# Performance work log

Measured on AMD Instinct MI355X. Metric: run time of the kernel, lower is better.

The kernel has to match this reference:

```python
import jax, jax.numpy as jnp
import numpy as np

B, L, DMQ, DMV = 8, 1024, 512, 512
H, DK, DV, DOUT = 8, 64, 64, 512
EPS = 1e-6


def _layer_norm(x, gamma, beta):
    # LayerNorm over last dim (size H*DK or H*DV), eps=1e-6
    mu = jnp.mean(x, axis=-1, keepdims=True)
    var = jnp.mean(jnp.square(x - mu), axis=-1, keepdims=True)
    return (x - mu) * jax.lax.rsqrt(var + EPS) * gamma + beta


def setup_inputs() -> dict:
    key = jax.random.key(0)
    ks = jax.random.split(key, 20)
    s = 0.02
    return {
        "q": jax.random.normal(ks[0], (B, L, DMQ), jnp.float32),
        "k": jax.random.normal(ks[1], (B, L, DMV), jnp.float32),
        "v": jax.random.normal(ks[2], (B, L, DMV), jnp.float32),
        "Wq": jax.random.normal(ks[3], (DMQ, H * DK), jnp.float32) * s,
        "bq": jnp.zeros((H * DK,), jnp.float32),
        "Wk": jax.random.normal(ks[4], (DMV, H * DK), jnp.float32) * s,
        "bk": jnp.zeros((H * DK,), jnp.float32),
        "Wv": jax.random.normal(ks[5], (DMV, H * DV), jnp.float32) * s,
        "bv": jnp.zeros((H * DV,), jnp.float32),
        "g_q": jnp.ones((H * DK,), jnp.float32),
        "be_q": jnp.zeros((H * DK,), jnp.float32),
        "g_k": jnp.ones((H * DK,), jnp.float32),
        "be_k": jnp.zeros((H * DK,), jnp.float32),
        "g_v": jnp.ones((H * DV,), jnp.float32),
        "be_v": jnp.zeros((H * DV,), jnp.float32),
        "W1": jax.random.normal(ks[6], (H * DV, H * DV), jnp.float32) * s,
        "b1": jnp.zeros((H * DV,), jnp.float32),
        "W2": jax.random.normal(ks[7], (H * DV, DOUT), jnp.float32) * s,
        "b2": jnp.zeros((DOUT,), jnp.float32),
    }


def reference(q, k, v, Wq, bq, Wk, bk, Wv, bv, g_q, be_q, g_k, be_k, g_v, be_v, W1, b1, W2, b2):
    b, lq = q.shape[0], q.shape[1]
    qp = q @ Wq + bq                       # [B, Lq, H*DK]
    kp = k @ Wk + bk                       # [B, Lk, H*DK]
    vp = v @ Wv + bv                       # [B, Lv, H*DV]
    residual = qp.reshape(b, lq, H, DK)
    qn = _layer_norm(qp, g_q, be_q).reshape(b, lq, H, DK)
    kn = _layer_norm(kp, g_k, be_k).reshape(b, -1, H, DK)
    vn = _layer_norm(vp, g_v, be_v).reshape(b, -1, H, DV)
    # scaled dot-product attention (mask=None path)
    scores = jnp.einsum("bqhd,bkhd->bhqk", qn, kn) / jnp.sqrt(jnp.float32(DK))
    attn = jax.nn.softmax(scores, axis=-1)
    out = jnp.einsum("bhqk,bkhd->bqhd", attn, vn).reshape(b, lq, H * DV)
    # 2-layer FFN head: fc1 (ReLU) then fc2
    h = jax.nn.relu(out @ W1 + b1)
    out = h @ W2 + b2                      # [B, Lq, DOUT]
    return (out, residual)
```

## Files before the change

kernel.cpp:

```cpp
#include <hip/hip_runtime.h>
#include <hip/hip_bf16.h>
#include <stdint.h>

typedef unsigned short u16;
typedef __attribute__((ext_vector_type(8))) short bf16x8;
typedef __attribute__((ext_vector_type(4))) float f32x4;
typedef __attribute__((ext_vector_type(16))) float f32x16;

#define NR 8192
#define DM 512
#define NH 8
#define HD 64
#define LQ 1024

#define QSCALE (0.125f * 1.4426950408889634f)
#define SOFF 16.0f

__device__ __forceinline__ u16 f2b(float f) {
    union { float f; uint32_t u; } v; v.f = f;
    uint32_t r = v.u + 0x7fffu + ((v.u >> 16) & 1u);
    return (u16)(r >> 16);
}
__device__ __forceinline__ uint32_t pk2(float lo, float hi) {
    __hip_bfloat162 h = __float22bfloat162_rn(make_float2(lo, hi));
    union { __hip_bfloat162 h; uint32_t u; } c; c.h = h;
    return c.u;
}

__global__ __launch_bounds__(256)
void conv3_kernel(const float* __restrict__ q, const float* __restrict__ k,
                  const float* __restrict__ v, u16* __restrict__ qo,
                  u16* __restrict__ ko, u16* __restrict__ vo)
{
    const int y = blockIdx.y;
    const float* in = y == 0 ? q : y == 1 ? k : v;
    u16* out = y == 0 ? qo : y == 1 ? ko : vo;
    const int i = blockIdx.x * 256 + threadIdx.x;
    const float4* p = (const float4*)in + (size_t)i * 2;
    float4 a = p[0], b = p[1];
    uint4 o;
    o.x = pk2(a.x, a.y);
    o.y = pk2(a.z, a.w);
    o.z = pk2(b.x, b.y);
    o.w = pk2(b.z, b.w);
    ((uint4*)out)[i] = o;
}

__global__ __launch_bounds__(256)
void wt5_kernel(const float* __restrict__ W0, const float* __restrict__ W1,
                const float* __restrict__ W2, const float* __restrict__ W3,
                const float* __restrict__ W4,
                u16* __restrict__ T0, u16* __restrict__ T1, u16* __restrict__ T2,
                u16* __restrict__ T3, u16* __restrict__ T4)
{
    const int z = blockIdx.z;
    const float* W = z == 0 ? W0 : z == 1 ? W1 : z == 2 ? W2 : z == 3 ? W3 : W4;
    u16* Wt = z == 0 ? T0 : z == 1 ? T1 : z == 2 ? T2 : z == 3 ? T3 : T4;

    __shared__ float S[64][65];
    const int k0 = blockIdx.x * 64, n0 = blockIdx.y * 64;
    #pragma unroll
    for (int p = 0; p < 16; ++p) {
        int idx = threadIdx.x + p * 256;
        int r = idx >> 6, c = idx & 63;
        S[r][c] = W[(size_t)(k0 + r) * DM + n0 + c];
    }
    __syncthreads();
    #pragma unroll
    for (int p = 0; p < 16; ++p) {
        int idx = threadIdx.x + p * 256;
        int r = idx >> 6, c = idx & 63;
        Wt[(size_t)(n0 + r) * DM + k0 + c] = f2b(S[c][r]);
    }
}

__global__ __launch_bounds__(256)
void vt_kernel(const u16* __restrict__ vn, u16* __restrict__ vt)
{
    __shared__ u16 S[64][82];
    const int lt = blockIdx.x, bh = blockIdx.y;
    const int b = bh >> 3, h = bh & 7;
    const int t = threadIdx.x;
    {
        const int r = t >> 2, dc = (t & 3) * 16;
        const u16* src = vn + (size_t)(b * LQ + lt * 64 + r) * DM + h * HD + dc;
        *(uint4*)&S[r][dc]     = *(const uint4*)(src);
        *(uint4*)&S[r][dc + 8] = *(const uint4*)(src + 8);
    }
    __syncthreads();
    {
        const int d = t >> 2, lc = (t & 3) * 16;
        u16 tmp[16];
        #pragma unroll
        for (int e = 0; e < 16; ++e) tmp[e] = S[lc + e][d];
        u16* dst = vt + (((size_t)bh * HD + d) << 10) + lt * 64 + lc;
        *(uint4*)dst       = *(uint4*)&tmp[0];
        *(uint4*)(dst + 8) = *(uint4*)&tmp[8];
    }
}

__global__ __launch_bounds__(256)
void ln3_kernel(const float* __restrict__ Pq, const float* __restrict__ Pk,
                const float* __restrict__ Pv,
                const float* __restrict__ gq, const float* __restrict__ bq,
                const float* __restrict__ gk, const float* __restrict__ bk,
                const float* __restrict__ gv, const float* __restrict__ bv,
                u16* __restrict__ oq, u16* __restrict__ ok, u16* __restrict__ ov)
{
    const int y = blockIdx.y;
    const float* P  = y == 0 ? Pq : y == 1 ? Pk : Pv;
    const float* gm = y == 0 ? gq : y == 1 ? gk : gv;
    const float* be = y == 0 ? bq : y == 1 ? bk : bv;
    u16* out = y == 0 ? oq : y == 1 ? ok : ov;
    const float scale = y == 0 ? QSCALE : 1.f;

    const int row = blockIdx.x, t = threadIdx.x;
    const size_t off = (size_t)row * DM + t * 2;
    float2 v = *(const float2*)(P + off);
    float s = v.x + v.y, s2 = v.x * v.x + v.y * v.y;
    #pragma unroll
    for (int o = 32; o; o >>= 1) { s += __shfl_down(s, o); s2 += __shfl_down(s2, o); }
    __shared__ float ss[4], ss2[4];
    if ((t & 63) == 0) { ss[t >> 6] = s; ss2[t >> 6] = s2; }
    __syncthreads();
    float S = ss[0] + ss[1] + ss[2] + ss[3];
    float S2 = ss2[0] + ss2[1] + ss2[2] + ss2[3];
    float mu = S * (1.f / DM);
    float var = S2 * (1.f / DM) - mu * mu;
    float rs = rsqrtf(var + 1e-6f);
    float g0 = gm[t * 2] * scale, g1 = gm[t * 2 + 1] * scale;
    float b0 = be[t * 2] * scale, b1 = be[t * 2 + 1] * scale;
    float o0 = (v.x - mu) * rs * g0 + b0;
    float o1 = (v.y - mu) * rs * g1 + b1;
    *(uint32_t*)(out + off) = pk2(o0, o1);
}

template<bool RELU, bool OUT_BF16>
__device__ __forceinline__
void gemm_body(const u16* __restrict__ A, const u16* __restrict__ Bt,
               const float* __restrict__ bias, void* __restrict__ Cout)
{
    __shared__ u16 Al[4 * 128 * 8];
    __shared__ u16 Bl[4 * 128 * 8];
    const int t = threadIdx.x;
    const int w = t >> 6, l = t & 63;
    const int m0 = blockIdx.x * 128, n0 = blockIdx.y * 128;
    const int sg = w & 3, sr = (w >> 2) * 64;
    const int wm = w >> 2, wn = w & 3;

    const u16* Ap = A  + (size_t)(m0 + sr + l) * DM + sg * 8;
    const u16* Bp = Bt + (size_t)(n0 + sr + l) * DM + sg * 8;
    const int su = (sg * 128 + sr + l) * 8;

    uint4 ga = *(const uint4*)Ap;
    uint4 gb = *(const uint4*)Bp;

    f32x4 acc[4][2];
    #pragma unroll
    for (int mi = 0; mi < 4; ++mi)
        #pragma unroll
        for (int ni = 0; ni < 2; ++ni)
            acc[mi][ni] = {0.f, 0.f, 0.f, 0.f};

    for (int kb = 0; kb < DM / 32; ++kb) {
        __syncthreads();
        *(uint4*)&Al[su] = ga;
        *(uint4*)&Bl[su] = gb;
        if (kb + 1 < DM / 32) {
            ga = *(const uint4*)(Ap + (kb + 1) * 32);
            gb = *(const uint4*)(Bp + (kb + 1) * 32);
        }
        __syncthreads();
        bf16x8 af[4], bfr[2];
        #pragma unroll
        for (int mi = 0; mi < 4; ++mi)
            af[mi] = *(const bf16x8*)&Al[((l >> 4) * 128 + wm * 64 + mi * 16 + (l & 15)) * 8];
        #pragma unroll
        for (int ni = 0; ni < 2; ++ni)
            bfr[ni] = *(const bf16x8*)&Bl[((l >> 4) * 128 + wn * 32 + ni * 16 + (l & 15)) * 8];
        #pragma unroll
        for (int mi = 0; mi < 4; ++mi)
            #pragma unroll
            for (int ni = 0; ni < 2; ++ni)
                acc[mi][ni] = __builtin_amdgcn_mfma_f32_16x16x32_bf16(af[mi], bfr[ni], acc[mi][ni], 0, 0, 0);
    }

    const int cq = l >> 4, cr = l & 15;
    #pragma unroll
    for (int mi = 0; mi < 4; ++mi) {
        const int row = m0 + wm * 64 + mi * 16 + cq * 4;
        #pragma unroll
        for (int ni = 0; ni < 2; ++ni) {
            const int col = n0 + wn * 32 + ni * 16 + cr;
            const float bb = bias[col];
            #pragma unroll
            for (int j = 0; j < 4; ++j) {
                float vv = acc[mi][ni][j] + bb;
                if (RELU) vv = fmaxf(vv, 0.f);
                if (OUT_BF16) ((u16*)Cout)[(size_t)(row + j) * DM + col] = f2b(vv);
                else          ((float*)Cout)[(size_t)(row + j) * DM + col] = vv;
            }
        }
    }
}

template<bool RELU, bool OUT_BF16>
__global__ __launch_bounds__(512)
void mfma_gemm_kernel(const u16* __restrict__ A, const u16* __restrict__ Bt,
                      const float* __restrict__ bias, void* __restrict__ Cout)
{
    gemm_body<RELU, OUT_BF16>(A, Bt, bias, Cout);
}

__global__ __launch_bounds__(512)
void gemm_qkv_kernel(const u16* __restrict__ qbf, const u16* __restrict__ kbf,
                     const u16* __restrict__ vbf,
                     const u16* __restrict__ WqT, const u16* __restrict__ WkT,
                     const u16* __restrict__ WvT,
                     const float* __restrict__ bq, const float* __restrict__ bk,
                     const float* __restrict__ bv,
                     float* __restrict__ res, float* __restrict__ kp,
                     float* __restrict__ vp)
{
    const int z = blockIdx.z;
    const u16* A    = z == 0 ? qbf : z == 1 ? kbf : vbf;
    const u16* Bt   = z == 0 ? WqT : z == 1 ? WkT : WvT;
    const float* bb = z == 0 ? bq  : z == 1 ? bk  : bv;
    void* C         = z == 0 ? (void*)res : z == 1 ? (void*)kp : (void*)vp;
    gemm_body<false, false>(A, Bt, bb, C);
}

__global__ __launch_bounds__(256, 3)
void attn_mfma_kernel(const u16* __restrict__ qn, const u16* __restrict__ kn,
                      const u16* __restrict__ vt, u16* __restrict__ ab)
{
    __shared__ u16 Kl[2][8 * 64 * 8];
    __shared__ u16 Vl[2][8 * 64 * 8];
    __shared__ u16 Pl[4][8 * 32 * 8];

    const int t = threadIdx.x;
    const int w = t >> 6, l = t & 63;
    const int hi = l >> 5, ln = l & 31;

    const int bid = blockIdx.x;
    const int slot = bid >> 3;
    const int bh = (bid & 7) + 8 * (slot & 7);
    const int qt = slot >> 3;
    const int b = bh >> 3, h = bh & 7;

    const size_t bbase = (size_t)b * LQ * DM + h * HD;
    const int q0 = qt * 128 + w * 32;

    bf16x8 qf[4];
    {
        const u16* qp = qn + bbase + (size_t)(q0 + ln) * DM + hi * 8;
        #pragma unroll
        for (int c = 0; c < 4; ++c)
            qf[c] = *(const bf16x8*)(qp + c * 16);
    }

    const u16* Kg = kn + bbase + (size_t)(t & 63) * DM + (t >> 6) * 8;
    const u16* Vg = vt + (((size_t)bh * HD + (t >> 3)) << 10) + (t & 7) * 8;
    const int svu1 = ((t & 7) * 64 + (t >> 3)) * 8;
    const int svu2 = ((t & 7) * 64 + 32 + (t >> 3)) * 8;
    u16* Pw = &Pl[w][0];

    f32x16 oa0, oa1;
    #pragma unroll
    for (int r = 0; r < 16; ++r) { oa0[r] = 0.f; oa1[r] = 0.f; }
    float lsum = 0.f;

    *(uint4*)&Kl[0][t * 8]         = *(const uint4*)Kg;
    *(uint4*)&Kl[0][(t + 256) * 8] = *(const uint4*)(Kg + 32);
    *(uint4*)&Vl[0][svu1]          = *(const uint4*)Vg;
    *(uint4*)&Vl[0][svu2]          = *(const uint4*)(Vg + (32 << 10));
    uint4 ka1 = *(const uint4*)(Kg + (size_t)64 * DM);
    uint4 ka2 = *(const uint4*)(Kg + (size_t)64 * DM + 32);
    uint4 va1 = *(const uint4*)(Vg + 64);
    uint4 va2 = *(const uint4*)(Vg + (32 << 10) + 64);
    int cur = 0;

    for (int kt = 0; kt < 16; ++kt) {
        __syncthreads();

        f32x16 sa0, sa1;
        #pragma unroll
        for (int r = 0; r < 16; ++r) { sa0[r] = -SOFF; sa1[r] = -SOFF; }
        #pragma unroll
        for (int c = 0; c < 4; ++c) {
            bf16x8 k0 = *(const bf16x8*)&Kl[cur][((c * 2 + hi) * 64 + ln) * 8];
            bf16x8 k1 = *(const bf16x8*)&Kl[cur][((c * 2 + hi) * 64 + 32 + ln) * 8];
            sa0 = __builtin_amdgcn_mfma_f32_32x32x16_bf16(k0, qf[c], sa0, 0, 0, 0);
            sa1 = __builtin_amdgcn_mfma_f32_32x32x16_bf16(k1, qf[c], sa1, 0, 0, 0);
        }

        if (kt < 15) {
            *(uint4*)&Kl[cur ^ 1][t * 8]         = ka1;
            *(uint4*)&Kl[cur ^ 1][(t + 256) * 8] = ka2;
            *(uint4*)&Vl[cur ^ 1][svu1]          = va1;
            *(uint4*)&Vl[cur ^ 1][svu2]          = va2;
            if (kt < 14) {
                ka1 = *(const uint4*)(Kg + (size_t)(kt + 2) * 64 * DM);
                ka2 = *(const uint4*)(Kg + (size_t)(kt + 2) * 64 * DM + 32);
                va1 = *(const uint4*)(Vg + (kt + 2) * 64);
                va2 = *(const uint4*)(Vg + (32 << 10) + (kt + 2) * 64);
            }
        }

        #pragma unroll
        for (int r = 0; r < 16; ++r) {
            sa0[r] = __builtin_amdgcn_exp2f(sa0[r]);
            sa1[r] = __builtin_amdgcn_exp2f(sa1[r]);
            lsum += sa0[r] + sa1[r];
        }

        #pragma unroll
        for (int g0 = 0; g0 < 4; ++g0) {
            uint2 w0, w1;
            w0.x = pk2(sa0[4 * g0],     sa0[4 * g0 + 1]);
            w0.y = pk2(sa0[4 * g0 + 2], sa0[4 * g0 + 3]);
            w1.x = pk2(sa1[4 * g0],     sa1[4 * g0 + 1]);
            w1.y = pk2(sa1[4 * g0 + 2], sa1[4 * g0 + 3]);
            *(uint2*)&Pw[(g0 * 32 + ln) * 8 + 4 * hi]       = w0;
            *(uint2*)&Pw[((g0 + 4) * 32 + ln) * 8 + 4 * hi] = w1;
        }

        #pragma unroll
        for (int ks = 0; ks < 4; ++ks) {
            bf16x8 pa = *(const bf16x8*)&Pw[((ks * 2 + hi) * 32 + ln) * 8];
            bf16x8 v0 = *(const bf16x8*)&Vl[cur][((ks * 2 + hi) * 64 + ln) * 8];
            bf16x8 v1 = *(const bf16x8*)&Vl[cur][((ks * 2 + hi) * 64 + 32 + ln) * 8];
            oa0 = __builtin_amdgcn_mfma_f32_32x32x16_bf16(v0, pa, oa0, 0, 0, 0);
            oa1 = __builtin_amdgcn_mfma_f32_32x32x16_bf16(v1, pa, oa1, 0, 0, 0);
        }
        cur ^= 1;
    }

    lsum += __shfl_xor(lsum, 32, 64);
    const float rinv = 1.f / lsum;
    u16* op = ab + (size_t)(b * LQ + q0 + ln) * DM + h * HD;
    #pragma unroll
    for (int g = 0; g < 4; ++g) {
        uint2 s0, s1;
        s0.x = pk2(oa0[4 * g] * rinv, oa0[4 * g + 1] * rinv);
        s0.y = pk2(oa0[4 * g + 2] * rinv, oa0[4 * g + 3] * rinv);
        s1.x = pk2(oa1[4 * g] * rinv, oa1[4 * g + 1] * rinv);
        s1.y = pk2(oa1[4 * g + 2] * rinv, oa1[4 * g + 3] * rinv);
        *(uint2*)(op + 8 * g + 4 * hi)      = s0;
        *(uint2*)(op + 32 + 8 * g + 4 * hi) = s1;
    }
}

extern "C" void kernel_launch(void* const* d_in, const int* in_sizes, int n_in,
                              void* d_out, int out_size, void* d_ws, size_t ws_size,
                              hipStream_t stream)
{
    const float* q    = (const float*)d_in[0];
    const float* k    = (const float*)d_in[1];
    const float* v    = (const float*)d_in[2];
    const float* Wq   = (const float*)d_in[3];
    const float* bq   = (const float*)d_in[4];
    const float* Wk   = (const float*)d_in[5];
    const float* bk   = (const float*)d_in[6];
    const float* Wv   = (const float*)d_in[7];
    const float* bv   = (const float*)d_in[8];
    const float* g_q  = (const float*)d_in[9];
    const float* be_q = (const float*)d_in[10];
    const float* g_k  = (const float*)d_in[11];
    const float* be_k = (const float*)d_in[12];
    const float* g_v  = (const float*)d_in[13];
    const float* be_v = (const float*)d_in[14];
    const float* W1   = (const float*)d_in[15];
    const float* b1   = (const float*)d_in[16];
    const float* W2   = (const float*)d_in[17];
    const float* b2   = (const float*)d_in[18];

    float* outp = (float*)d_out;
    float* res  = outp + (size_t)NR * DM;

    char* wsb = (char*)d_ws;
    const size_t MB = 1024 * 1024;
    float* kp  = (float*)(wsb);
    float* vp  = (float*)(wsb + 16 * MB);
    u16* qbf = (u16*)(wsb + 32 * MB);
    u16* kbf = (u16*)(wsb + 40 * MB);
    u16* vbf = (u16*)(wsb + 48 * MB);
    u16* WqT = (u16*)(wsb + 56 * MB);
    u16* WkT = WqT + 512 * 512;
    u16* WvT = WkT + 512 * 512;
    u16* W1T = WvT + 512 * 512;
    u16* W2T = W1T + 512 * 512;
    u16* abb = (u16*)kp;
    u16* hbb = (u16*)vp;
    u16* vtb = (u16*)(wsb + 24 * MB);

    conv3_kernel<<<dim3(2048, 3), 256, 0, stream>>>(q, k, v, qbf, kbf, vbf);

    wt5_kernel<<<dim3(8, 8, 5), 256, 0, stream>>>(Wq, Wk, Wv, W1, W2,
                                                  WqT, WkT, WvT, W1T, W2T);

    gemm_qkv_kernel<<<dim3(NR / 128, DM / 128, 3), 512, 0, stream>>>(
        qbf, kbf, vbf, WqT, WkT, WvT, bq, bk, bv, res, kp, vp);

    ln3_kernel<<<dim3(NR, 3), 256, 0, stream>>>(res, kp, vp,
                                                g_q, be_q, g_k, be_k, g_v, be_v,
                                                qbf, kbf, vbf);

    vt_kernel<<<dim3(16, 64), 256, 0, stream>>>(vbf, vtb);

    attn_mfma_kernel<<<512, 256, 0, stream>>>(qbf, kbf, vtb, abb);

    dim3 gg(NR / 128, DM / 128);
    mfma_gemm_kernel<true,  true ><<<gg, 512, 0, stream>>>(abb, W1T, b1, (void*)hbb);
    mfma_gemm_kernel<false, false><<<gg, 512, 0, stream>>>(hbb, W2T, b2, (void*)outp);
}
```

Baseline: 127.7 us.

## Fuse FFN layers into one kernel, merge prep kernels, store K/V projections as bf16

Replaces the two separate FFN GEMM launches with a single kernel. Each block computes a 32-row tile of the fc1 output, applies bias and ReLU, keeps it in shared memory as bf16, and then runs fc2 on it, so the hidden activation never goes through global memory. The input conversion and weight transpose kernels are merged into one launch. The K and V projections are now written as bf16 instead of fp32, which halves the traffic into the LayerNorm kernel. The trade-offs are a large shared-memory footprint, reloading full weight matrices per 32-row block, and a little extra rounding before the K/V LayerNorm.

After: 188.0 us. 47.2% more time.

```diff
diff --git a/kernel.cpp b/kernel.cpp
--- a/kernel.cpp
+++ b/kernel.cpp
@@ -26,51 +26,54 @@
     union { __hip_bfloat162 h; uint32_t u; } c; c.h = h;
     return c.u;
 }
+__device__ __forceinline__ float b2f(uint32_t lo16) {
+    union { uint32_t u; float f; } c; c.u = lo16 << 16; return c.f;
+}
 
 __global__ __launch_bounds__(256)
-void conv3_kernel(const float* __restrict__ q, const float* __restrict__ k,
-                  const float* __restrict__ v, u16* __restrict__ qo,
-                  u16* __restrict__ ko, u16* __restrict__ vo)
-{
-    const int y = blockIdx.y;
-    const float* in = y == 0 ? q : y == 1 ? k : v;
-    u16* out = y == 0 ? qo : y == 1 ? ko : vo;
-    const int i = blockIdx.x * 256 + threadIdx.x;
-    const float4* p = (const float4*)in + (size_t)i * 2;
-    float4 a = p[0], b = p[1];
-    uint4 o;
-    o.x = pk2(a.x, a.y);
-    o.y = pk2(a.z, a.w);
-    o.z = pk2(b.x, b.y);
-    o.w = pk2(b.z, b.w);
-    ((uint4*)out)[i] = o;
-}
-
-__global__ __launch_bounds__(256)
-void wt5_kernel(const float* __restrict__ W0, const float* __restrict__ W1,
-                const float* __restrict__ W2, const float* __restrict__ W3,
-                const float* __restrict__ W4,
-                u16* __restrict__ T0, u16* __restrict__ T1, u16* __restrict__ T2,
-                u16* __restrict__ T3, u16* __restrict__ T4)
-{
-    const int z = blockIdx.z;
-    const float* W = z == 0 ? W0 : z == 1 ? W1 : z == 2 ? W2 : z == 3 ? W3 : W4;
-    u16* Wt = z == 0 ? T0 : z == 1 ? T1 : z == 2 ? T2 : z == 3 ? T3 : T4;
-
+void prep_kernel(const float* __restrict__ q, const float* __restrict__ k,
+                 const float* __restrict__ v, u16* __restrict__ qo,
+                 u16* __restrict__ ko, u16* __restrict__ vo,
+                 const float* __restrict__ W0, const float* __restrict__ W1,
+                 const float* __restrict__ W2, const float* __restrict__ W3,
+                 const float* __restrict__ W4,
+                 u16* __restrict__ T0, u16* __restrict__ T1, u16* __restrict__ T2,
+                 u16* __restrict__ T3, u16* __restrict__ T4)
+{
     __shared__ float S[64][65];
-    const int k0 = blockIdx.x * 64, n0 = blockIdx.y * 64;
-    #pragma unroll
-    for (int p = 0; p < 16; ++p) {
-        int idx = threadIdx.x + p * 256;
-        int r = idx >> 6, c = idx & 63;
-        S[r][c] = W[(size_t)(k0 + r) * DM + n0 + c];
-    }
-    __syncthreads();
-    #pragma unroll
-    for (int p = 0; p < 16; ++p) {
-        int idx = threadIdx.x + p * 256;
-        int r = idx >> 6, c = idx & 63;
-        Wt[(size_t)(n0 + r) * DM + k0 + c] = f2b(S[c][r]);
+    const int bid = blockIdx.x;
+    if (bid < 6144) {
+        const int y = bid >> 11, x = bid & 2047;
+        const float* in = y == 0 ? q : y == 1 ? k : v;
+        u16* out = y == 0 ? qo : y == 1 ? ko : vo;
+        const int i = x * 256 + threadIdx.x;
+        const float4* p = (const float4*)in + (size_t)i * 2;
+        float4 a = p[0], b = p[1];
+        uint4 o;
+        o.x = pk2(a.x, a.y);
+        o.y = pk2(a.z, a.w);
+        o.z = pk2(b.x, b.y);
+        o.w = pk2(b.z, b.w);
+        ((uint4*)out)[i] = o;
+    } else {
+        const int id = bid - 6144;
+        const int z = id >> 6, idx = id & 63;
+        const float* W = z == 0 ? W0 : z == 1 ? W1 : z == 2 ? W2 : z == 3 ? W3 : W4;
+        u16* Wt = z == 0 ? T0 : z == 1 ? T1 : z == 2 ? T2 : z == 3 ? T3 : T4;
+        const int k0 = (idx >> 3) * 64, n0 = (idx & 7) * 64;
+        #pragma unroll
+        for (int p = 0; p < 16; ++p) {
+            int i = threadIdx.x + p * 256;
+            int r = i >> 6, c = i & 63;
+            S[r][c] = W[(size_t)(k0 + r) * DM + n0 + c];
+        }
+        __syncthreads();
+        #pragma unroll
+        for (int p = 0; p < 16; ++p) {
+            int i = threadIdx.x + p * 256;
+            int r = i >> 6, c = i & 63;
+            Wt[(size_t)(n0 + r) * DM + k0 + c] = f2b(S[c][r]);
+        }
     }
 }
 
@@ -100,15 +103,14 @@
 }
 
 __global__ __launch_bounds__(256)
-void ln3_kernel(const float* __restrict__ Pq, const float* __restrict__ Pk,
-                const float* __restrict__ Pv,
+void ln3_kernel(const float* __restrict__ Pq, const u16* __restrict__ Pk,
+                const u16* __restrict__ Pv,
                 const float* __restrict__ gq, const float* __restrict__ bq,
                 const float* __restrict__ gk, const float* __restrict__ bk,
                 const float* __restrict__ gv, const float* __restrict__ bv,
                 u16* __restrict__ oq, u16* __restrict__ ok, u16* __restrict__ ov)
 {
     const int y = blockIdx.y;
-    const float* P  = y == 0 ? Pq : y == 1 ? Pk : Pv;
     const float* gm = y == 0 ? gq : y == 1 ? gk : gv;
     const float* be = y == 0 ? bq : y == 1 ? bk : bv;
     u16* out = y == 0 ? oq : y == 1 ? ok : ov;
@@ -116,8 +118,16 @@
 
     const int row = blockIdx.x, t = threadIdx.x;
     const size_t off = (size_t)row * DM + t * 2;
-    float2 v = *(const float2*)(P + off);
-    float s = v.x + v.y, s2 = v.x * v.x + v.y * v.y;
+    float vx, vy;
+    if (y == 0) {
+        float2 v = *(const float2*)(Pq + off);
+        vx = v.x; vy = v.y;
+    } else {
+        const u16* P = y == 1 ? Pk : Pv;
+        uint32_t u = *(const uint32_t*)(P + off);
+        vx = b2f(u & 0xffffu); vy = b2f(u >> 16);
+    }
+    float s = vx + vy, s2 = vx * vx + vy * vy;
     #pragma unroll
     for (int o = 32; o; o >>= 1) { s += __shfl_down(s, o); s2 += __shfl_down(s2, o); }
     __shared__ float ss[4], ss2[4];
@@ -130,86 +140,9 @@
     float rs = rsqrtf(var + 1e-6f);
     float g0 = gm[t * 2] * scale, g1 = gm[t * 2 + 1] * scale;
     float b0 = be[t * 2] * scale, b1 = be[t * 2 + 1] * scale;
-    float o0 = (v.x - mu) * rs * g0 + b0;
-    float o1 = (v.y - mu) * rs * g1 + b1;
+    float o0 = (vx - mu) * rs * g0 + b0;
+    float o1 = (vy - mu) * rs * g1 + b1;
     *(uint32_t*)(out + off) = pk2(o0, o1);
-}
-
-template<bool RELU, bool OUT_BF16>
-__device__ __forceinline__
-void gemm_body(const u16* __restrict__ A, const u16* __restrict__ Bt,
-               const float* __restrict__ bias, void* __restrict__ Cout)
-{
-    __shared__ u16 Al[4 * 128 * 8];
-    __shared__ u16 Bl[4 * 128 * 8];
-    const int t = threadIdx.x;
-    const int w = t >> 6, l = t & 63;
-    const int m0 = blockIdx.x * 128, n0 = blockIdx.y * 128;
-    const int sg = w & 3, sr = (w >> 2) * 64;
-    const int wm = w >> 2, wn = w & 3;
-
-    const u16* Ap = A  + (size_t)(m0 + sr + l) * DM + sg * 8;
-    const u16* Bp = Bt + (size_t)(n0 + sr + l) * DM + sg * 8;
-    const int su = (sg * 128 + sr + l) * 8;
-
-    uint4 ga = *(const uint4*)Ap;
-    uint4 gb = *(const uint4*)Bp;
-
-    f32x4 acc[4][2];
-    #pragma unroll
-    for (int mi = 0; mi < 4; ++mi)
-        #pragma unroll
-        for (int ni = 0; ni < 2; ++ni)
-            acc[mi][ni] = {0.f, 0.f, 0.f, 0.f};
-
-    for (int kb = 0; kb < DM / 32; ++kb) {
-        __syncthreads();
-        *(uint4*)&Al[su] = ga;
-        *(uint4*)&Bl[su] = gb;
-        if (kb + 1 < DM / 32) {
-            ga = *(const uint4*)(Ap + (kb + 1) * 32);
-            gb = *(const uint4*)(Bp + (kb + 1) * 32);
-        }
-        __syncthreads();
-        bf16x8 af[4], bfr[2];
-        #pragma unroll
-        for (int mi = 0; mi < 4; ++mi)
-            af[mi] = *(const bf16x8*)&Al[((l >> 4) * 128 + wm * 64 + mi * 16 + (l & 15)) * 8];
-        #pragma unroll
-        for (int ni = 0; ni < 2; ++ni)
-            bfr[ni] = *(const bf16x8*)&Bl[((l >> 4) * 128 + wn * 32 + ni * 16 + (l & 15)) * 8];
-        #pragma unroll
-        for (int mi = 0; mi < 4; ++mi)
-            #pragma unroll
-            for (int ni = 0; ni < 2; ++ni)
-                acc[mi][ni] = __builtin_amdgcn_mfma_f32_16x16x32_bf16(af[mi], bfr[ni], acc[mi][ni], 0, 0, 0);
-    }
-
-    const int cq = l >> 4, cr = l & 15;
-    #pragma unroll
-    for (int mi = 0; mi < 4; ++mi) {
-        const int row = m0 + wm * 64 + mi * 16 + cq * 4;
-        #pragma unroll
-        for (int ni = 0; ni < 2; ++ni) {
-            const int col = n0 + wn * 32 + ni * 16 + cr;
-            const float bb = bias[col];
-            #pragma unroll
-            for (int j = 0; j < 4; ++j) {
-                float vv = acc[mi][ni][j] + bb;
-                if (RELU) vv = fmaxf(vv, 0.f);
-                if (OUT_BF16) ((u16*)Cout)[(size_t)(row + j) * DM + col] = f2b(vv);
-                else          ((float*)Cout)[(size_t)(row + j) * DM + col] = vv;
-            }
-        }
-    }
-}
-
-template<bool RELU, bool OUT_BF16>
-__global__ __launch_bounds__(512)
-void mfma_gemm_kernel(const u16* __restrict__ A, const u16* __restrict__ Bt,
-                      const float* __restrict__ bias, void* __restrict__ Cout)
-{
-    gemm_body<RELU, OUT_BF16>(A, Bt, bias, Cout);
 }
 
 __global__ __launch_bounds__(512)
@@ -219,15 +152,218 @@
                      const u16* __restrict__ WvT,
                      const float* __restrict__ bq, const float* __restrict__ bk,
                      const float* __restrict__ bv,
-                     float* __restrict__ res, float* __restrict__ kp,
-                     float* __restrict__ vp)
-{
+                     float* __restrict__ res, u16* __restrict__ kpb,
+                     u16* __restrict__ vpb)
+{
+    __shared__ u16 Al[4 * 128 * 8];
+    __shared__ u16 Bl[4 * 128 * 8];
     const int z = blockIdx.z;
     const u16* A    = z == 0 ? qbf : z == 1 ? kbf : vbf;
     const u16* Bt   = z == 0 ? WqT : z == 1 ? WkT : WvT;
     const float* bb = z == 0 ? bq  : z == 1 ? bk  : bv;
-    void* C         = z == 0 ? (void*)res : z == 1 ? (void*)kp : (void*)vp;
-    gemm_body<false, false>(A, Bt, bb, C);
+    const bool obf  = z != 0;
+    u16* ob   = z == 1 ? kpb : vpb;
+
+    const int t = threadIdx.x;
+    const int w = t >> 6, l = t & 63;
+    const int m0 = blockIdx.x * 128, n0 = blockIdx.y * 128;
+    const int sg = w & 3, sr = (w >> 2) * 64;
+    const int wm = w >> 2, wn = w & 3;
+
+    const u16* Ap = A  + (size_t)(m0 + sr + l) * DM + sg * 8;
+    const u16* Bp = Bt + (size_t)(n0 + sr + l) * DM + sg * 8;
+    const int su = (sg * 128 + sr + l) * 8;
+
+    uint4 ga = *(const uint4*)Ap;
+    uint4 gb = *(const uint4*)Bp;
+
+    f32x4 acc[4][2];
+    #pragma unroll
+    for (int mi = 0; mi < 4; ++mi)
+        #pragma unroll
+        for (int ni = 0; ni < 2; ++ni)
+            acc[mi][ni] = {0.f, 0.f, 0.f, 0.f};
+
+    for (int kb = 0; kb < DM / 32; ++kb) {
+        __syncthreads();
+        *(uint4*)&Al[su] = ga;
+        *(uint4*)&Bl[su] = gb;
+        if (kb + 1 < DM / 32) {
+            ga = *(const uint4*)(Ap + (kb + 1) * 32);
+            gb = *(const uint4*)(Bp + (kb + 1) * 32);
+        }
+        __syncthreads();
+        bf16x8 af[4], bfr[2];
+        #pragma unroll
+        for (int mi = 0; mi < 4; ++mi)
+            af[mi] = *(const bf16x8*)&Al[((l >> 4) * 128 + wm * 64 + mi * 16 + (l & 15)) * 8];
+        #pragma unroll
+        for (int ni = 0; ni < 2; ++ni)
+            bfr[ni] = *(const bf16x8*)&Bl[((l >> 4) * 128 + wn * 32 + ni * 16 + (l & 15)) * 8];
+        #pragma unroll
+        for (int mi = 0; mi < 4; ++mi)
+            #pragma unroll
+            for (int ni = 0; ni < 2; ++ni)
+                acc[mi][ni] = __builtin_amdgcn_mfma_f32_16x16x32_bf16(af[mi], bfr[ni], acc[mi][ni], 0, 0, 0);
+    }
+
+    const int cq = l >> 4, cr = l & 15;
+    #pragma unroll
+    for (int mi = 0; mi < 4; ++mi) {
+        const int row = m0 + wm * 64 + mi * 16 + cq * 4;
+        #pragma unroll
+        for (int ni = 0; ni < 2; ++ni) {
+            const int col = n0 + wn * 32 + ni * 16 + cr;
+            const float bbv = bb[col];
+            #pragma unroll
+            for (int j = 0; j < 4; ++j) {
+                float vv = acc[mi][ni][j] + bbv;
+                if (obf) ob[(size_t)(row + j) * DM + col] = f2b(vv);
+                else     res[(size_t)(row + j) * DM + col] = vv;
+            }
+        }
+    }
+}
+
+__global__ __launch_bounds__(256, 2)
+void ffn_kernel(const u16* __restrict__ A, const u16* __restrict__ W1T,
+                const float* __restrict__ b1, const u16* __restrict__ W2T,
+                const float* __restrict__ b2, float* __restrict__ out)
+{
+    __shared__ u16 Bl[4 * 512 * 8];
+    __shared__ u16 Al[4 * 32 * 8];
+    __shared__ u16 Hl[64 * 32 * 8];
+
+    const int t = threadIdx.x;
+    const int w = t >> 6, l = t & 63;
+    const int m0 = blockIdx.x * 32;
+    const int wn = w;
+    const int cq = l >> 4, cr = l & 15;
+
+    const u16* B1p  = W1T + (size_t)t * DM;
+    const u16* B1p2 = W1T + (size_t)(t + 256) * DM;
+    const u16* B2p  = W2T + (size_t)t * DM;
+    const u16* B2p2 = W2T + (size_t)(t + 256) * DM;
+    const u16* Ap   = A + (size_t)(m0 + (t & 31)) * DM + (t >> 5) * 8;
+
+    float b1c[8], b2c[8];
+    #pragma unroll
+    for (int ni = 0; ni < 8; ++ni) {
+        b1c[ni] = b1[wn * 128 + ni * 16 + cr];
+        b2c[ni] = b2[wn * 128 + ni * 16 + cr];
+    }
+
+    f32x4 acc[2][8];
+    #pragma unroll
+    for (int mi = 0; mi < 2; ++mi)
+        #pragma unroll
+        for (int ni = 0; ni < 8; ++ni)
+            acc[mi][ni] = {0.f, 0.f, 0.f, 0.f};
+
+    uint4 gb[8]; uint4 ga;
+    #pragma unroll
+    for (int p = 0; p < 4; ++p) {
+        gb[p]     = *(const uint4*)(B1p  + p * 8);
+        gb[4 + p] = *(const uint4*)(B1p2 + p * 8);
+    }
+    if (t < 128) ga = *(const uint4*)Ap;
+
+    for (int kb = 0; kb < 16; ++kb) {
+        __syncthreads();
+        #pragma unroll
+        for (int p = 0; p < 4; ++p) {
+            *(uint4*)&Bl[(p * 512 + t) * 8]       = gb[p];
+            *(uint4*)&Bl[(p * 512 + t + 256) * 8] = gb[4 + p];
+        }
+        if (t < 128) *(uint4*)&Al[t * 8] = ga;
+        if (kb + 1 < 16) {
+            #pragma unroll
+            for (int p = 0; p < 4; ++p) {
+                gb[p]     = *(const uint4*)(B1p  + (kb + 1) * 32 + p * 8);
+                gb[4 + p] = *(const uint4*)(B1p2 + (kb + 1) * 32 + p * 8);
+            }
+            if (t < 128) ga = *(const uint4*)(Ap + (kb + 1) * 32);
+        }
+        __syncthreads();
+        bf16x8 af[2], bfr[8];
+        #pragma unroll
+        for (int mi = 0; mi < 2; ++mi)
+            af[mi] = *(const bf16x8*)&Al[((l >> 4) * 32 + mi * 16 + (l & 15)) * 8];
+        #pragma unroll
+        for (int ni = 0; ni < 8; ++ni)
+            bfr[ni] = *(const bf16x8*)&Bl[((l >> 4) * 512 + wn * 128 + ni * 16 + (l & 15)) * 8];
+        #pragma unroll
+        for (int mi = 0; mi < 2; ++mi)
+            #pragma unroll
+            for (int ni = 0; ni < 8; ++ni)
+                acc[mi][ni] = __builtin_amdgcn_mfma_f32_16x16x32_bf16(af[mi], bfr[ni], acc[mi][ni], 0, 0, 0);
+    }
+
+    #pragma unroll
+    for (int p = 0; p < 4; ++p) {
+        gb[p]     = *(const uint4*)(B2p  + p * 8);
+        gb[4 + p] = *(const uint4*)(B2p2 + p * 8);
+    }
+
+    #pragma unroll
+    for (int mi = 0; mi < 2; ++mi)
+        #pragma unroll
+        for (int j = 0; j < 4; ++j) {
+            const int r = mi * 16 + cq * 4 + j;
+            #pragma unroll
+            for (int ni = 0; ni < 8; ++ni) {
+                const int c = wn * 128 + ni * 16 + cr;
+                float hv = fmaxf(acc[mi][ni][j] + b1c[ni], 0.f);
+                Hl[((c >> 3) * 32 + r) * 8 + (c & 7)] = f2b(hv);
+            }
+        }
+
+    #pragma unroll
+    for (int mi = 0; mi < 2; ++mi)
+        #pragma unroll
+        for (int ni = 0; ni < 8; ++ni)
+            acc[mi][ni] = {0.f, 0.f, 0.f, 0.f};
+
+    for (int kb = 0; kb < 16; ++kb) {
+        __syncthreads();
+        #pragma unroll
+        for (int p = 0; p < 4; ++p) {
+            *(uint4*)&Bl[(p * 512 + t) * 8]       = gb[p];
+            *(uint4*)&Bl[(p * 512 + t + 256) * 8] = gb[4 + p];
+        }
+        if (kb + 1 < 16) {
+            #pragma unroll
+            for (int p = 0; p < 4; ++p) {
+                gb[p]     = *(const uint4*)(B2p  + (kb + 1) * 32 + p * 8);
+                gb[4 + p] = *(const uint4*)(B2p2 + (kb + 1) * 32 + p * 8);
+            }
+        }
+        __syncthreads();
+        bf16x8 af[2], bfr[8];
+        #pragma unroll
+        for (int mi = 0; mi < 2; ++mi)
+            af[mi] = *(const bf16x8*)&Hl[(((kb * 4 + (l >> 4)) * 32) + mi * 16 + (l & 15)) * 8];
+        #pragma unroll
+        for (int ni = 0; ni < 8; ++ni)
+            bfr[ni] = *(const bf16x8*)&Bl[((l >> 4) * 512 + wn * 128 + ni * 16 + (l & 15)) * 8];
+        #pragma unroll
+        for (int mi = 0; mi < 2; ++mi)
+            #pragma unroll
+            for (int ni = 0; ni < 8; ++ni)
+                acc[mi][ni] = __builtin_amdgcn_mfma_f32_16x16x32_bf16(af[mi], bfr[ni], acc[mi][ni], 0, 0, 0);
+    }
+
+    #pragma unroll
+    for (int mi = 0; mi < 2; ++mi)
+        #pragma unroll
+        for (int j = 0; j < 4; ++j) {
+            const int r = m0 + mi * 16 + cq * 4 + j;
+            #pragma unroll
+            for (int ni = 0; ni < 8; ++ni) {
+                const int c = wn * 128 + ni * 16 + cr;
+                out[(size_t)r * DM + c] = acc[mi][ni][j] + b2c[ni];
+            }
+        }
 }
 
 __global__ __launch_bounds__(256, 3)
@@ -380,8 +516,9 @@
 
     char* wsb = (char*)d_ws;
     const size_t MB = 1024 * 1024;
-    float* kp  = (float*)(wsb);
-    float* vp  = (float*)(wsb + 16 * MB);
+    u16* kpb = (u16*)(wsb);
+    u16* vpb = (u16*)(wsb + 8 * MB);
+    u16* vtb = (u16*)(wsb + 24 * MB);
     u16* qbf = (u16*)(wsb + 32 * MB);
     u16* kbf = (u16*)(wsb + 40 * MB);
     u16* vbf = (u16*)(wsb + 48 * MB);
@@ -390,19 +527,16 @@
     u16* WvT = WkT + 512 * 512;
     u16* W1T = WvT + 512 * 512;
     u16* W2T = W1T + 512 * 512;
-    u16* abb = (u16*)kp;
-    u16* hbb = (u16*)vp;
-    u16* vtb = (u16*)(wsb + 24 * MB);
-
-    conv3_kernel<<<dim3(2048, 3), 256, 0, stream>>>(q, k, v, qbf, kbf, vbf);
-
-    wt5_kernel<<<dim3(8, 8, 5), 256, 0, stream>>>(Wq, Wk, Wv, W1, W2,
-                                                  WqT, WkT, WvT, W1T, W2T);
+    u16* abb = (u16*)wsb;
+
+    prep_kernel<<<6464, 256, 0, stream>>>(q, k, v, qbf, kbf, vbf,
+                                          Wq, Wk, Wv, W1, W2,
+                                          WqT, WkT, WvT, W1T, W2T);
 
     gemm_qkv_kernel<<<dim3(NR / 128, DM / 128, 3), 512, 0, stream>>>(
-        qbf, kbf, vbf, WqT, WkT, WvT, bq, bk, bv, res, kp, vp);
-
-    ln3_kernel<<<dim3(NR, 3), 256, 0, stream>>>(res, kp, vp,
+        qbf, kbf, vbf, WqT, WkT, WvT, bq, bk, bv, res, kpb, vpb);
+
+    ln3_kernel<<<dim3(NR, 3), 256, 0, stream>>>(res, kpb, vpb,
                                                 g_q, be_q, g_k, be_k, g_v, be_v,
                                                 qbf, kbf, vbf);
 
@@ -410,7 +544,5 @@
 
     attn_mfma_kernel<<<512, 256, 0, stream>>>(qbf, kbf, vtb, abb);
 
-    dim3 gg(NR / 128, DM / 128);
-    mfma_gemm_kernel<true,  true ><<<gg, 512, 0, stream>>>(abb, W1T, b1, (void*)hbb);
-    mfma_gemm_kernel<false, false><<<gg, 512, 0, stream>>>(hbb, W2T, b2, (void*)outp);
-}
+    ffn_kernel<<<NR / 32, 256, 0, stream>>>(abb, W1T, b1, W2T, b2, outp);
+}
```

## Store K/V projections as bf16 and merge input conversion with weight transpose

Applied to the files above, without the earlier changes.

The QKV projection GEMM now writes the K and V projections as bf16 instead of fp32, while Q stays fp32 because it is the residual output. LayerNorm reads them back as bf16, which cuts intermediate write and read traffic for two of the three streams. The separate input-conversion and weight-transpose kernels are merged into one launch to save launch overhead. Rounding K/V to bf16 before LayerNorm adds some precision loss, and the GEMM body is duplicated inline with a per-element branch in the epilogue.

New measurement: 123.7 us. -3.2%, faster.

```diff
diff --git a/kernel.cpp b/kernel.cpp
--- a/kernel.cpp
+++ b/kernel.cpp
@@ -26,51 +26,54 @@
     union { __hip_bfloat162 h; uint32_t u; } c; c.h = h;
     return c.u;
 }
+__device__ __forceinline__ float b2f(uint32_t lo16) {
+    union { uint32_t u; float f; } c; c.u = lo16 << 16; return c.f;
+}
 
 __global__ __launch_bounds__(256)
-void conv3_kernel(const float* __restrict__ q, const float* __restrict__ k,
-                  const float* __restrict__ v, u16* __restrict__ qo,
-                  u16* __restrict__ ko, u16* __restrict__ vo)
-{
-    const int y = blockIdx.y;
-    const float* in = y == 0 ? q : y == 1 ? k : v;
-    u16* out = y == 0 ? qo : y == 1 ? ko : vo;
-    const int i = blockIdx.x * 256 + threadIdx.x;
-    const float4* p = (const float4*)in + (size_t)i * 2;
-    float4 a = p[0], b = p[1];
-    uint4 o;
-    o.x = pk2(a.x, a.y);
-    o.y = pk2(a.z, a.w);
-    o.z = pk2(b.x, b.y);
-    o.w = pk2(b.z, b.w);
-    ((uint4*)out)[i] = o;
-}
-
-__global__ __launch_bounds__(256)
-void wt5_kernel(const float* __restrict__ W0, const float* __restrict__ W1,
-                const float* __restrict__ W2, const float* __restrict__ W3,
-                const float* __restrict__ W4,
-                u16* __restrict__ T0, u16* __restrict__ T1, u16* __restrict__ T2,
-                u16* __restrict__ T3, u16* __restrict__ T4)
-{
-    const int z = blockIdx.z;
-    const float* W = z == 0 ? W0 : z == 1 ? W1 : z == 2 ? W2 : z == 3 ? W3 : W4;
-    u16* Wt = z == 0 ? T0 : z == 1 ? T1 : z == 2 ? T2 : z == 3 ? T3 : T4;
-
+void prep_kernel(const float* __restrict__ q, const float* __restrict__ k,
+                 const float* __restrict__ v, u16* __restrict__ qo,
+                 u16* __restrict__ ko, u16* __restrict__ vo,
+                 const float* __restrict__ W0, const float* __restrict__ W1,
+                 const float* __restrict__ W2, const float* __restrict__ W3,
+                 const float* __restrict__ W4,
+                 u16* __restrict__ T0, u16* __restrict__ T1, u16* __restrict__ T2,
+                 u16* __restrict__ T3, u16* __restrict__ T4)
+{
     __shared__ float S[64][65];
-    const int k0 = blockIdx.x * 64, n0 = blockIdx.y * 64;
-    #pragma unroll
-    for (int p = 0; p < 16; ++p) {
-        int idx = threadIdx.x + p * 256;
-        int r = idx >> 6, c = idx & 63;
-        S[r][c] = W[(size_t)(k0 + r) * DM + n0 + c];
-    }
-    __syncthreads();
-    #pragma unroll
-    for (int p = 0; p < 16; ++p) {
-        int idx = threadIdx.x + p * 256;
-        int r = idx >> 6, c = idx & 63;
-        Wt[(size_t)(n0 + r) * DM + k0 + c] = f2b(S[c][r]);
+    const int bid = blockIdx.x;
+    if (bid < 6144) {
+        const int y = bid >> 11, x = bid & 2047;
+        const float* in = y == 0 ? q : y == 1 ? k : v;
+        u16* out = y == 0 ? qo : y == 1 ? ko : vo;
+        const int i = x * 256 + threadIdx.x;
+        const float4* p = (const float4*)in + (size_t)i * 2;
+        float4 a = p[0], b = p[1];
+        uint4 o;
+        o.x = pk2(a.x, a.y);
+        o.y = pk2(a.z, a.w);
+        o.z = pk2(b.x, b.y);
+        o.w = pk2(b.z, b.w);
+        ((uint4*)out)[i] = o;
+    } else {
+        const int id = bid - 6144;
+        const int z = id >> 6, idx = id & 63;
+        const float* W = z == 0 ? W0 : z == 1 ? W1 : z == 2 ? W2 : z == 3 ? W3 : W4;
+        u16* Wt = z == 0 ? T0 : z == 1 ? T1 : z == 2 ? T2 : z == 3 ? T3 : T4;
+        const int k0 = (idx >> 3) * 64, n0 = (idx & 7) * 64;
+        #pragma unroll
+        for (int p = 0; p < 16; ++p) {
+            int i = threadIdx.x + p * 256;
+            int r = i >> 6, c = i & 63;
+            S[r][c] = W[(size_t)(k0 + r) * DM + n0 + c];
+        }
+        __syncthreads();
+        #pragma unroll
+        for (int p = 0; p < 16; ++p) {
+            int i = threadIdx.x + p * 256;
+            int r = i >> 6, c = i & 63;
+            Wt[(size_t)(n0 + r) * DM + k0 + c] = f2b(S[c][r]);
+        }
     }
 }
 
@@ -100,15 +103,14 @@
 }
 
 __global__ __launch_bounds__(256)
-void ln3_kernel(const float* __restrict__ Pq, const float* __restrict__ Pk,
-                const float* __restrict__ Pv,
+void ln3_kernel(const float* __restrict__ Pq, const u16* __restrict__ Pk,
+                const u16* __restrict__ Pv,
                 const float* __restrict__ gq, const float* __restrict__ bq,
                 const float* __restrict__ gk, const float* __restrict__ bk,
                 const float* __restrict__ gv, const float* __restrict__ bv,
                 u16* __restrict__ oq, u16* __restrict__ ok, u16* __restrict__ ov)
 {
     const int y = blockIdx.y;
-    const float* P  = y == 0 ? Pq : y == 1 ? Pk : Pv;
     const float* gm = y == 0 ? gq : y == 1 ? gk : gv;
     const float* be = y == 0 ? bq : y == 1 ? bk : bv;
     u16* out = y == 0 ? oq : y == 1 ? ok : ov;
@@ -116,8 +118,16 @@
 
     const int row = blockIdx.x, t = threadIdx.x;
     const size_t off = (size_t)row * DM + t * 2;
-    float2 v = *(const float2*)(P + off);
-    float s = v.x + v.y, s2 = v.x * v.x + v.y * v.y;
+    float vx, vy;
+    if (y == 0) {
+        float2 v = *(const float2*)(Pq + off);
+        vx = v.x; vy = v.y;
+    } else {
+        const u16* P = y == 1 ? Pk : Pv;
+        uint32_t u = *(const uint32_t*)(P + off);
+        vx = b2f(u & 0xffffu); vy = b2f(u >> 16);
+    }
+    float s = vx + vy, s2 = vx * vx + vy * vy;
     #pragma unroll
     for (int o = 32; o; o >>= 1) { s += __shfl_down(s, o); s2 += __shfl_down(s2, o); }
     __shared__ float ss[4], ss2[4];
@@ -130,8 +140,8 @@
     float rs = rsqrtf(var + 1e-6f);
     float g0 = gm[t * 2] * scale, g1 = gm[t * 2 + 1] * scale;
     float b0 = be[t * 2] * scale, b1 = be[t * 2 + 1] * scale;
-    float o0 = (v.x - mu) * rs * g0 + b0;
-    float o1 = (v.y - mu) * rs * g1 + b1;
+    float o0 = (vx - mu) * rs * g0 + b0;
+    float o1 = (vy - mu) * rs * g1 + b1;
     *(uint32_t*)(out + off) = pk2(o0, o1);
 }
 
@@ -219,15 +229,77 @@
                      const u16* __restrict__ WvT,
                      const float* __restrict__ bq, const float* __restrict__ bk,
                      const float* __restrict__ bv,
-                     float* __restrict__ res, float* __restrict__ kp,
-                     float* __restrict__ vp)
-{
+                     float* __restrict__ res, u16* __restrict__ kpb,
+                     u16* __restrict__ vpb)
+{
+    __shared__ u16 Al[4 * 128 * 8];
+    __shared__ u16 Bl[4 * 128 * 8];
     const int z = blockIdx.z;
     const u16* A    = z == 0 ? qbf : z == 1 ? kbf : vbf;
     const u16* Bt   = z == 0 ? WqT : z == 1 ? WkT : WvT;
     const float* bb = z == 0 ? bq  : z == 1 ? bk  : bv;
-    void* C         = z == 0 ? (void*)res : z == 1 ? (void*)kp : (void*)vp;
-    gemm_body<false, false>(A, Bt, bb, C);
+    const bool obf  = z != 0;
+    u16* ob   = z == 1 ? kpb : vpb;
+
+    const int t = threadIdx.x;
+    const int w = t >> 6, l = t & 63;
+    const int m0 = blockIdx.x * 128, n0 = blockIdx.y * 128;
+    const int sg = w & 3, sr = (w >> 2) * 64;
+    const int wm = w >> 2, wn = w & 3;
+
+    const u16* Ap = A  + (size_t)(m0 + sr + l) * DM + sg * 8;
+    const u16* Bp = Bt + (size_t)(n0 + sr + l) * DM + sg * 8;
+    const int su = (sg * 128 + sr + l) * 8;
+
+    uint4 ga = *(const uint4*)Ap;
+    uint4 gb = *(const uint4*)Bp;
+
+    f32x4 acc[4][2];
+    #pragma unroll
+    for (int mi = 0; mi < 4; ++mi)
+        #pragma unroll
+        for (int ni = 0; ni < 2; ++ni)
+            acc[mi][ni] = {0.f, 0.f, 0.f, 0.f};
+
+    for (int kb = 0; kb < DM / 32; ++kb) {
+        __syncthreads();
+        *(uint4*)&Al[su] = ga;
+        *(uint4*)&Bl[su] = gb;
+        if (kb + 1 < DM / 32) {
+            ga = *(const uint4*)(Ap + (kb + 1) * 32);
+            gb = *(const uint4*)(Bp + (kb + 1) * 32);
+        }
+        __syncthreads();
+        bf16x8 af[4], bfr[2];
+        #pragma unroll
+        for (int mi = 0; mi < 4; ++mi)
+            af[mi] = *(const bf16x8*)&Al[((l >> 4) * 128 + wm * 64 + mi * 16 + (l & 15)) * 8];
+        #pragma unroll
+        for (int ni = 0; ni < 2; ++ni)
+            bfr[ni] = *(const bf16x8*)&Bl[((l >> 4) * 128 + wn * 32 + ni * 16 + (l & 15)) * 8];
+        #pragma unroll
+        for (int mi = 0; mi < 4; ++mi)
+            #pragma unroll
+            for (int ni = 0; ni < 2; ++ni)
+                acc[mi][ni] = __builtin_amdgcn_mfma_f32_16x16x32_bf16(af[mi], bfr[ni], acc[mi][ni], 0, 0, 0);
+    }
+
+    const int cq = l >> 4, cr = l & 15;
+    #pragma unroll
+    for (int mi = 0; mi < 4; ++mi) {
+        const int row = m0 + wm * 64 + mi * 16 + cq * 4;
+        #pragma unroll
+        for (int ni = 0; ni < 2; ++ni) {
+            const int col = n0 + wn * 32 + ni * 16 + cr;
+            const float bbv = bb[col];
+            #pragma unroll
+            for (int j = 0; j < 4; ++j) {
+                float vv = acc[mi][ni][j] + bbv;
+                if (obf) ob[(size_t)(row + j) * DM + col] = f2b(vv);
+                else     res[(size_t)(row + j) * DM + col] = vv;
+            }
+        }
+    }
 }
 
 __global__ __launch_bounds__(256, 3)
@@ -380,8 +452,10 @@
 
     char* wsb = (char*)d_ws;
     const size_t MB = 1024 * 1024;
-    float* kp  = (float*)(wsb);
-    float* vp  = (float*)(wsb + 16 * MB);
+    u16* kpb = (u16*)(wsb);
+    u16* vpb = (u16*)(wsb + 8 * MB);
+    u16* hbb = (u16*)(wsb + 16 * MB);
+    u16* vtb = (u16*)(wsb + 24 * MB);
     u16* qbf = (u16*)(wsb + 32 * MB);
     u16* kbf = (u16*)(wsb + 40 * MB);
     u16* vbf = (u16*)(wsb + 48 * MB);
@@ -390,19 +464,16 @@
     u16* WvT = WkT + 512 * 512;
     u16* W1T = WvT + 512 * 512;
     u16* W2T = W1T + 512 * 512;
-    u16* abb = (u16*)kp;
-    u16* hbb = (u16*)vp;
-    u16* vtb = (u16*)(wsb + 24 * MB);
-
-    conv3_kernel<<<dim3(2048, 3), 256, 0, stream>>>(q, k, v, qbf, kbf, vbf);
-
-    wt5_kernel<<<dim3(8, 8, 5), 256, 0, stream>>>(Wq, Wk, Wv, W1, W2,
-                                                  WqT, WkT, WvT, W1T, W2T);
+    u16* abb = (u16*)wsb;
+
+    prep_kernel<<<6464, 256, 0, stream>>>(q, k, v, qbf, kbf, vbf,
+                                          Wq, Wk, Wv, W1, W2,
+                                          WqT, WkT, WvT, W1T, W2T);
 
     gemm_qkv_kernel<<<dim3(NR / 128, DM / 128, 3), 512, 0, stream>>>(
-        qbf, kbf, vbf, WqT, WkT, WvT, bq, bk, bv, res, kp, vp);
-
-    ln3_kernel<<<dim3(NR, 3), 256, 0, stream>>>(res, kp, vp,
+        qbf, kbf, vbf, WqT, WkT, WvT, bq, bk, bv, res, kpb, vpb);
+
+    ln3_kernel<<<dim3(NR, 3), 256, 0, stream>>>(res, kpb, vpb,
                                                 g_q, be_q, g_k, be_k, g_v, be_v,
                                                 qbf, kbf, vbf);
 
```
